# Kernel tuning notes

Hardware: AMD Instinct MI355X
Metric: run time of the kernel (lower is better)

## Reference

```python
import jax, jax.numpy as jnp
import numpy as np

V, L, H, D, DFF = 32000, 6, 8, 64, 1024
DM = H * D  # 512
N, T = 4, 1024
EPS = 1e-3  # keras LayerNormalization default epsilon


def setup_inputs() -> dict:
    key = jax.random.key(0)
    ks = jax.random.split(key, 13)
    s = 0.02
    return {
        "x": jax.random.randint(ks[0], (N, T), 0, V, dtype=jnp.int32),
        "emb": jax.random.normal(ks[1], (V, DM), jnp.float32) * s,
        "Wqkv": jax.random.normal(ks[2], (L, DM, 3 * DM), jnp.float32) * s,
        "bqkv": jnp.zeros((L, 3 * DM), jnp.float32),
        "Wff": jax.random.normal(ks[3], (L, DM, DFF), jnp.float32) * s,
        "bff": jnp.zeros((L, DFF), jnp.float32),
        "Wo": jax.random.normal(ks[4], (L, DFF, DM), jnp.float32) * s,
        "bo": jnp.zeros((L, DM), jnp.float32),
        "g1": jnp.ones((L, DM), jnp.float32),
        "beta1": jnp.zeros((L, DM), jnp.float32),
        "g2": jnp.ones((L, DM), jnp.float32),
        "beta2": jnp.zeros((L, DM), jnp.float32),
    }


def _pos_encoding(seq_len, d_model):
    pos = jnp.arange(seq_len, dtype=jnp.float32)[:, None]
    i = jnp.arange(d_model, dtype=jnp.float32)[None, :]
    angle_rates = 1.0 / jnp.power(10000.0, 2.0 * jnp.floor(i / 2.0) / d_model)
    ang = pos * angle_rates
    even = (jnp.arange(d_model) % 2) == 0
    return jnp.where(even[None, :], jnp.sin(ang), jnp.cos(ang))  # [T, DM]


def _ln(x, g, b):
    m = jnp.mean(x, axis=-1, keepdims=True)
    v = jnp.mean(jnp.square(x - m), axis=-1, keepdims=True)
    return g * (x - m) / jnp.sqrt(v + EPS) + b


def reference(x, emb, Wqkv, bqkv, Wff, bff, Wo, bo, g1, beta1, g2, beta2):
    n, t = x.shape
    h = emb[x] * jnp.sqrt(jnp.float32(DM))          # [N,T,DM]
    h = h + _pos_encoding(t, DM)[None, :, :]
    # causal additive mask: 1 above diagonal, 0 on/below
    mask = 1.0 - jnp.tril(jnp.ones((t, t), jnp.float32))
    neg = mask[None, None, :, :] * -1e9
    scale = 1.0 / jnp.sqrt(jnp.float32(D))
    for l in range(L):
        qkv = h @ Wqkv[l] + bqkv[l]                 # [N,T,3*DM]
        qkv = qkv.reshape(n, t, H, D, 3)
        q, k, v = [jnp.transpose(qkv[..., j], (0, 2, 1, 3)) for j in range(3)]  # [N,H,T,D]
        logits = jnp.einsum("nhtd,nhsd->nhts", q, k) * scale + neg
        w = jax.nn.softmax(logits, axis=-1)
        a = jnp.einsum("nhts,nhsd->nhtd", w, v)     # [N,H,T,D]
        a = jnp.transpose(a, (0, 2, 1, 3)).reshape(n, t, DM)
        h = _ln(h + a, g1[l], beta1[l])
        ff = jax.nn.relu(h @ Wff[l] + bff[l]) @ Wo[l] + bo[l]
        h = _ln(h + ff, g2[l], beta2[l])
    return h
```

## Files before the change

kernel.cpp:

```cpp
#include <hip/hip_runtime.h>
#include <hip/hip_bf16.h>
#include <math.h>

#define DM   512
#define TT   1024
#define NB   4
#define NHD  8
#define LAYERS 6
#define DFFD 1024
#define MROWS (NB*TT)
#define PERBUF (NB*NHD*TT*64)

typedef __bf16 bf16x8 __attribute__((ext_vector_type(8)));
typedef __bf16 bf16x4 __attribute__((ext_vector_type(4)));
typedef float f32x4 __attribute__((ext_vector_type(4)));

__device__ __forceinline__ void gl_lds16(const __bf16* g, __bf16* l) {
    __builtin_amdgcn_global_load_lds((const __attribute__((address_space(1))) void*)g,
                                     (__attribute__((address_space(3))) void*)l, 16, 0, 0);
}

__global__ __launch_bounds__(256) void embed_pos_kernel(const int* __restrict__ x,
    const float* __restrict__ emb, float* __restrict__ h, __bf16* __restrict__ hb)
{
    int row = blockIdx.x;
    int t = row & (TT - 1);
    int tok = x[row];
    const float* e = emb + (size_t)tok * DM;
    float* out = h + (size_t)row * DM;
    __bf16* outb = hb + (size_t)row * DM;
    for (int i = threadIdx.x; i < DM; i += 256) {
        float val = e[i] * 22.62741699796952f;
        int pair = i >> 1;
        float rate = powf(10000.0f, -(float)pair * (1.0f / 256.0f));
        float ang = (float)t * rate;
        float pe = (i & 1) ? cosf(ang) : sinf(ang);
        float v = val + pe;
        out[i] = v;
        outb[i] = (__bf16)v;
    }
}

__global__ __launch_bounds__(256) void convert_all_kernel(
    const float* __restrict__ Wqkv, const float* __restrict__ Wff, const float* __restrict__ Wo,
    const float* __restrict__ bqkv,
    __bf16* __restrict__ WtQ, __bf16* __restrict__ WtF, __bf16* __restrict__ WtO,
    float* __restrict__ bqkv_p)
{
    __shared__ float tile[32][33];
    int l = blockIdx.z;
    int t = blockIdx.x;
    const float* W; __bf16* Wt; int K, N, bx, by; bool perm = false;
    if (t < 768)       { W = Wqkv; Wt = WtQ; K = 512;  N = 1536; bx = t & 15;  by = t >> 4; perm = true; }
    else if (t < 1280) { int u = t - 768;  W = Wff; Wt = WtF; K = 512;  N = 1024; bx = u & 15; by = u >> 4; }
    else               { int u = t - 1280; W = Wo;  Wt = WtO; K = 1024; N = 512;  bx = u & 31; by = u >> 5; }
    int k0 = bx * 32, n0 = by * 32;
    const float* Wl = W + (size_t)l * K * N;
    __bf16* Wtl = Wt + (size_t)l * K * N;
    int tx = threadIdx.x & 31, ty = threadIdx.x >> 5;
    #pragma unroll
    for (int i = ty; i < 32; i += 8)
        tile[i][tx] = Wl[(size_t)(k0 + i) * N + n0 + tx];
    if (perm && bx == 0 && ty == 0) {
        int c = n0 + tx;
        bqkv_p[l * 1536 + (c % 3) * 512 + c / 3] = bqkv[(size_t)l * 1536 + c];
    }
    __syncthreads();
    #pragma unroll
    for (int i = ty; i < 32; i += 8) {
        int c = n0 + i;
        int row = perm ? ((c % 3) * 512 + c / 3) : c;
        Wtl[(size_t)row * K + k0 + tx] = (__bf16)tile[tx][i];
    }
}

__global__ __launch_bounds__(256) void gemm_mfma(const __bf16* __restrict__ A,
    const __bf16* __restrict__ Bt, const float* __restrict__ bias,
    __bf16* __restrict__ Cb, int M, int Nc, int K, int mode)
{
    __shared__ __align__(16) __bf16 As[2][128 * 32];
    __shared__ __align__(16) __bf16 Bs[2][128 * 32];
    int tid = threadIdx.x;
    int lane = tid & 63;
    int wave = tid >> 6;
    int ln = lane & 15, q = lane >> 4;
    int wrow = (wave >> 1) * 64, wcol = (wave & 1) * 64;
    int n0 = blockIdx.x * 128, m0 = blockIdx.y * 128;

    f32x4 acc[4][4] = {};

    const __bf16* Ab = A + (size_t)m0 * K;
    const __bf16* Bb = Bt + (size_t)n0 * K;

    int srow = lane >> 2;
    int scol = (lane & 3) * 8;
    const __bf16* Ag0 = Ab + (size_t)(wave * 32 + srow) * K + scol;
    const __bf16* Ag1 = Ab + (size_t)(wave * 32 + 16 + srow) * K + scol;
    const __bf16* Bg0 = Bb + (size_t)(wave * 32 + srow) * K + scol;
    const __bf16* Bg1 = Bb + (size_t)(wave * 32 + 16 + srow) * K + scol;

    for (int k0 = 0; k0 < K; k0 += 64) {
        __syncthreads();
        #pragma unroll
        for (int p = 0; p < 2; p++) {
            int kp = k0 + p * 32;
            gl_lds16(Ag0 + kp, As[p] + (wave * 32) * 32);
            gl_lds16(Ag1 + kp, As[p] + (wave * 32 + 16) * 32);
            gl_lds16(Bg0 + kp, Bs[p] + (wave * 32) * 32);
            gl_lds16(Bg1 + kp, Bs[p] + (wave * 32 + 16) * 32);
        }
        __syncthreads();

        #pragma unroll
        for (int p = 0; p < 2; p++) {
            bf16x8 af[4], bfr[4];
            #pragma unroll
            for (int mt = 0; mt < 4; mt++)
                af[mt] = *(const bf16x8*)&As[p][(wrow + mt * 16 + ln) * 32 + q * 8];
            #pragma unroll
            for (int nt = 0; nt < 4; nt++)
                bfr[nt] = *(const bf16x8*)&Bs[p][(wcol + nt * 16 + ln) * 32 + q * 8];
            #pragma unroll
            for (int mt = 0; mt < 4; mt++)
                #pragma unroll
                for (int nt = 0; nt < 4; nt++)
                    acc[mt][nt] = __builtin_amdgcn_mfma_f32_16x16x32_bf16(af[mt], bfr[nt], acc[mt][nt], 0, 0, 0);
        }
    }

    #pragma unroll
    for (int mt = 0; mt < 4; mt++) {
        int mbase = m0 + wrow + mt * 16 + q * 4;
        if (mode == 1) {
            #pragma unroll
            for (int r = 0; r < 4; r++) {
                int m = mbase + r;
                #pragma unroll
                for (int nt = 0; nt < 4; nt++) {
                    int c = n0 + wcol + nt * 16 + ln;
                    float val = acc[mt][nt][r] + bias[c];
                    Cb[(size_t)m * Nc + c] = (__bf16)fmaxf(val, 0.f);
                }
            }
        } else {
            int n = mbase >> 10, t = mbase & (TT - 1);
            #pragma unroll
            for (int nt = 0; nt < 4; nt++) {
                int c = n0 + wcol + nt * 16 + ln;
                int buf = c >> 9;
                int hd = c & 511;
                int hh = hd >> 6, d = hd & 63;
                float bv = bias[c];
                if (buf == 2) {
                    size_t idx = 2 * (size_t)PERBUF + (((size_t)(n * NHD + hh) * 64 + d) << 10) + t;
                    bf16x4 v4;
                    #pragma unroll
                    for (int r = 0; r < 4; r++) v4[r] = (__bf16)(acc[mt][nt][r] + bv);
                    *(bf16x4*)&Cb[idx] = v4;
                } else {
                    size_t base = (size_t)buf * PERBUF + (((size_t)(n * NHD + hh) * TT + t) << 6) + d;
                    #pragma unroll
                    for (int r = 0; r < 4; r++)
                        Cb[base + (size_t)(r << 6)] = (__bf16)(acc[mt][nt][r] + bv);
                }
            }
        }
    }
}

__global__ __launch_bounds__(256) void gemm_ff2(const __bf16* __restrict__ A,
    const __bf16* __restrict__ Bt, const float* __restrict__ bias,
    float* __restrict__ C, int M, int Nc, int K)
{
    __shared__ __align__(16) __bf16 As[2][128 * 32];
    __shared__ __align__(16) __bf16 Bs[2][64 * 32];
    int tid = threadIdx.x;
    int lane = tid & 63;
    int wave = tid >> 6;
    int ln = lane & 15, q = lane >> 4;
    int wrow = (wave >> 1) * 64, wcol = (wave & 1) * 32;
    int n0 = blockIdx.x * 64, m0 = blockIdx.y * 128;

    f32x4 acc[4][2] = {};

    const __bf16* Ab = A + (size_t)m0 * K;
    const __bf16* Bb = Bt + (size_t)n0 * K;

    int srow = lane >> 2;
    int scol = (lane & 3) * 8;
    const __bf16* Ag0 = Ab + (size_t)(wave * 32 + srow) * K + scol;
    const __bf16* Ag1 = Ab + (size_t)(wave * 32 + 16 + srow) * K + scol;
    const __bf16* Bg0 = Bb + (size_t)(wave * 16 + srow) * K + scol;

    for (int k0 = 0; k0 < K; k0 += 64) {
        __syncthreads();
        #pragma unroll
        for (int p = 0; p < 2; p++) {
            int kp = k0 + p * 32;
            gl_lds16(Ag0 + kp, As[p] + (wave * 32) * 32);
            gl_lds16(Ag1 + kp, As[p] + (wave * 32 + 16) * 32);
            gl_lds16(Bg0 + kp, Bs[p] + (wave * 16) * 32);
        }
        __syncthreads();

        #pragma unroll
        for (int p = 0; p < 2; p++) {
            bf16x8 af[4], bfr[2];
            #pragma unroll
            for (int mt = 0; mt < 4; mt++)
                af[mt] = *(const bf16x8*)&As[p][(wrow + mt * 16 + ln) * 32 + q * 8];
            #pragma unroll
            for (int nt = 0; nt < 2; nt++)
                bfr[nt] = *(const bf16x8*)&Bs[p][(wcol + nt * 16 + ln) * 32 + q * 8];
            #pragma unroll
            for (int mt = 0; mt < 4; mt++)
                #pragma unroll
                for (int nt = 0; nt < 2; nt++)
                    acc[mt][nt] = __builtin_amdgcn_mfma_f32_16x16x32_bf16(af[mt], bfr[nt], acc[mt][nt], 0, 0, 0);
        }
    }

    #pragma unroll
    for (int mt = 0; mt < 4; mt++) {
        #pragma unroll
        for (int r = 0; r < 4; r++) {
            int m = m0 + wrow + mt * 16 + q * 4 + r;
            #pragma unroll
            for (int nt = 0; nt < 2; nt++) {
                int c = n0 + wcol + nt * 16 + ln;
                C[(size_t)m * Nc + c] = acc[mt][nt][r] + bias[c];
            }
        }
    }
}

#define PPAD 72
#define NCHUNK 40
__global__ __launch_bounds__(256) void attn_partial_kernel(const __bf16* __restrict__ qb,
    const __bf16* __restrict__ kb, const __bf16* __restrict__ vtb,
    float* __restrict__ po, float* __restrict__ pden)
{
    __shared__ __align__(16) __bf16 Ksh[64 * 64];
    __shared__ __align__(16) __bf16 Vsh[2][64 * 64];
    __shared__ __align__(16) __bf16 Ps[64 * PPAD];

    int u = (NCHUNK - 1) - blockIdx.x;
    int nh = blockIdx.y;
    int g, off;
    if (u < 4)       { g = 0; off = 0;  }
    else if (u < 12) { g = 1; off = 4;  }
    else if (u < 24) { g = 2; off = 12; }
    else             { g = 3; off = 24; }
    int rem = u - off;
    int nper = g + 1;
    int qq = rem / nper;
    int c  = rem - qq * nper;
    int qt = g * 4 + qq;
    int st0 = c * 4;
    int st1 = min(st0 + 4, qt + 1);

    int tid = threadIdx.x;
    int lane = tid & 63, w = tid >> 6;
    int ln = lane & 15, q = lane >> 4;

    const __bf16* Kg = kb + (size_t)nh * TT * 64;
    const __bf16* Vg = vtb + (size_t)nh * 64 * TT;

    const __bf16* Qrow = qb + ((size_t)nh * TT + (size_t)qt * 64 + w * 16 + ln) * 64;
    bf16x8 aq0 = *(const bf16x8*)(Qrow + q * 8);
    bf16x8 aq1 = *(const bf16x8*)(Qrow + 32 + q * 8);

    int srow = lane >> 3;
    int swz  = ((lane & 7) ^ srow) << 3;
    int r0 = (w * 2 + 0) * 8 + srow;
    int r1 = (w * 2 + 1) * 8 + srow;
    const __bf16* Kg0 = Kg + (size_t)r0 * 64 + swz;
    const __bf16* Kg1 = Kg + (size_t)r1 * 64 + swz;
    const __bf16* Vg0 = Vg + (size_t)r0 * TT + swz;
    const __bf16* Vg1 = Vg + (size_t)r1 * TT + swz;
    __bf16* Kd0 = Ksh + (w * 2 + 0) * 512;
    __bf16* Kd1 = Ksh + (w * 2 + 1) * 512;

    f32x4 o_acc[4] = {};
    float den_reg[4] = {0.f, 0.f, 0.f, 0.f};

    int cur = 0;
    gl_lds16(Kg0 + st0 * 4096, Kd0);
    gl_lds16(Kg1 + st0 * 4096, Kd1);
    gl_lds16(Vg0 + st0 * 64, Vsh[0] + (w * 2 + 0) * 512);
    gl_lds16(Vg1 + st0 * 64, Vsh[0] + (w * 2 + 1) * 512);

    int kswz = ln & 7;
    for (int st = st0; st < st1; st++) {
        __syncthreads();

        f32x4 s_acc[4] = {};
        #pragma unroll
        for (int nt = 0; nt < 4; nt++) {
            int r = nt * 16 + ln;
            bf16x8 b0 = *(const bf16x8*)&Ksh[r * 64 + ((q ^ kswz) << 3)];
            s_acc[nt] = __builtin_amdgcn_mfma_f32_16x16x32_bf16(aq0, b0, s_acc[nt], 0, 0, 0);
            bf16x8 b1 = *(const bf16x8*)&Ksh[r * 64 + (((q + 4) ^ kswz) << 3)];
            s_acc[nt] = __builtin_amdgcn_mfma_f32_16x16x32_bf16(aq1, b1, s_acc[nt], 0, 0, 0);
        }

        bool diag = (st == qt);
        #pragma unroll
        for (int nt = 0; nt < 4; nt++) {
            #pragma unroll
            for (int r = 0; r < 4; r++) {
                int lrow = w * 16 + q * 4 + r;
                int lcol = nt * 16 + ln;
                float p;
                if (diag && lcol > lrow) p = 0.f;
                else p = exp2f(s_acc[nt][r] * 0.18033688011112042f);
                den_reg[r] += p;
                Ps[lrow * PPAD + lcol] = (__bf16)p;
            }
        }
        __syncthreads();

        if (st + 1 < st1) {
            gl_lds16(Kg0 + (st + 1) * 4096, Kd0);
            gl_lds16(Kg1 + (st + 1) * 4096, Kd1);
            gl_lds16(Vg0 + (st + 1) * 64, Vsh[cur ^ 1] + (w * 2 + 0) * 512);
            gl_lds16(Vg1 + (st + 1) * 64, Vsh[cur ^ 1] + (w * 2 + 1) * 512);
        }

        #pragma unroll
        for (int ks = 0; ks < 2; ks++) {
            bf16x8 af = *(const bf16x8*)&Vsh[cur][(w * 16 + ln) * 64 + (((ks * 4 + q) ^ kswz) << 3)];
            #pragma unroll
            for (int nt = 0; nt < 4; nt++) {
                bf16x8 bfr = *(const bf16x8*)&Ps[(nt * 16 + ln) * PPAD + ks * 32 + q * 8];
                o_acc[nt] = __builtin_amdgcn_mfma_f32_16x16x32_bf16(af, bfr, o_acc[nt], 0, 0, 0);
            }
        }
        cur ^= 1;
    }

    #pragma unroll
    for (int m = 1; m < 16; m <<= 1)
        #pragma unroll
        for (int r = 0; r < 4; r++)
            den_reg[r] += __shfl_xor(den_reg[r], m, 64);
    size_t slot = (size_t)nh * NCHUNK + u;
    if (ln == 0)
        #pragma unroll
        for (int r = 0; r < 4; r++)
            pden[slot * 64 + w * 16 + q * 4 + r] = den_reg[r];

    #pragma unroll
    for (int nt = 0; nt < 4; nt++)
        *(f32x4*)&po[(slot << 12) + (size_t)(nt * 16 + ln) * 64 + w * 16 + q * 4] = o_acc[nt];
}

__global__ __launch_bounds__(256) void add_ln_attn_kernel(float* __restrict__ h,
    __bf16* __restrict__ hb, const float* __restrict__ po, const float* __restrict__ pden,
    const float* __restrict__ g, const float* __restrict__ b)
{
    int w = threadIdx.x >> 6, lane = threadIdx.x & 63;
    int row = (blockIdx.x << 2) + w;
    int n = row >> 10, t = row & (TT - 1);
    int qt = t >> 6, qrow = t & 63;
    int gg = qt >> 2, nc = gg + 1;
    const int offs[4] = {0, 4, 12, 24};
    int u0 = offs[gg] + (qt - gg * 4) * nc;
    int hh = lane >> 3;
    int d0 = (lane & 7) * 8;
    size_t s0 = (size_t)(n * NHD + hh) * NCHUNK + u0;

    f32x4 a0 = {0.f,0.f,0.f,0.f}, a1 = {0.f,0.f,0.f,0.f};
    float den = 0.f;
    for (int c = 0; c < nc; c++) {
        const float* p = po + ((s0 + c) << 12) + (size_t)qrow * 64 + d0;
        a0 += *(const f32x4*)p;
        a1 += *(const f32x4*)(p + 4);
        den += pden[(s0 + c) * 64 + qrow];
    }
    float inv = 1.0f / den;

    size_t base = (size_t)row * DM + lane * 8;
    f32x4 x0 = *(const f32x4*)&h[base];
    f32x4 x1 = *(const f32x4*)&h[base + 4];
    x0 += a0 * inv;
    x1 += a1 * inv;

    float s1 = x0[0]+x0[1]+x0[2]+x0[3] + x1[0]+x1[1]+x1[2]+x1[3];
    float s2 = x0[0]*x0[0]+x0[1]*x0[1]+x0[2]*x0[2]+x0[3]*x0[3]
             + x1[0]*x1[0]+x1[1]*x1[1]+x1[2]*x1[2]+x1[3]*x1[3];
    #pragma unroll
    for (int m = 1; m < 64; m <<= 1) {
        s1 += __shfl_xor(s1, m, 64);
        s2 += __shfl_xor(s2, m, 64);
    }
    float mean = s1 * (1.0f / 512.0f);
    float var = s2 * (1.0f / 512.0f) - mean * mean;
    float rstd = rsqrtf(var + 1e-3f);

    f32x4 gg0 = *(const f32x4*)&g[lane * 8];
    f32x4 gg1 = *(const f32x4*)&g[lane * 8 + 4];
    f32x4 bb0 = *(const f32x4*)&b[lane * 8];
    f32x4 bb1 = *(const f32x4*)&b[lane * 8 + 4];
    f32x4 o0, o1;
    bf16x8 pb;
    #pragma unroll
    for (int i = 0; i < 4; i++) {
        o0[i] = gg0[i] * ((x0[i] - mean) * rstd) + bb0[i];
        o1[i] = gg1[i] * ((x1[i] - mean) * rstd) + bb1[i];
        pb[i] = (__bf16)o0[i];
        pb[4 + i] = (__bf16)o1[i];
    }
    *(f32x4*)&h[base] = o0;
    *(f32x4*)&h[base + 4] = o1;
    *(bf16x8*)(hb + base) = pb;
}

__global__ __launch_bounds__(256) void add_ln_kernel(float* __restrict__ h,
    __bf16* __restrict__ hb, const float* __restrict__ a,
    const float* __restrict__ g, const float* __restrict__ b)
{
    int w = threadIdx.x >> 6, lane = threadIdx.x & 63;
    int row = (blockIdx.x << 2) + w;
    size_t base4 = (size_t)row * (DM / 4);
    const float4* h4 = (const float4*)h;
    const float4* a4 = (const float4*)a;
    float4 x0 = h4[base4 + lane];
    float4 x1 = h4[base4 + 64 + lane];
    float4 y0 = a4[base4 + lane];
    float4 y1 = a4[base4 + 64 + lane];
    x0.x += y0.x; x0.y += y0.y; x0.z += y0.z; x0.w += y0.w;
    x1.x += y1.x; x1.y += y1.y; x1.z += y1.z; x1.w += y1.w;
    float s1 = x0.x + x0.y + x0.z + x0.w + x1.x + x1.y + x1.z + x1.w;
    float s2 = x0.x*x0.x + x0.y*x0.y + x0.z*x0.z + x0.w*x0.w
             + x1.x*x1.x + x1.y*x1.y + x1.z*x1.z + x1.w*x1.w;
    #pragma unroll
    for (int m = 1; m < 64; m <<= 1) {
        s1 += __shfl_xor(s1, m, 64);
        s2 += __shfl_xor(s2, m, 64);
    }
    float mean = s1 * (1.0f / 512.0f);
    float var = s2 * (1.0f / 512.0f) - mean * mean;
    float rstd = rsqrtf(var + 1e-3f);
    const float4* g4 = (const float4*)g;
    const float4* b4 = (const float4*)b;
    float4 gg0 = g4[lane], gg1 = g4[64 + lane];
    float4 bb0 = b4[lane], bb1 = b4[64 + lane];
    float4 o0, o1;
    o0.x = gg0.x * ((x0.x - mean) * rstd) + bb0.x;
    o0.y = gg0.y * ((x0.y - mean) * rstd) + bb0.y;
    o0.z = gg0.z * ((x0.z - mean) * rstd) + bb0.z;
    o0.w = gg0.w * ((x0.w - mean) * rstd) + bb0.w;
    o1.x = gg1.x * ((x1.x - mean) * rstd) + bb1.x;
    o1.y = gg1.y * ((x1.y - mean) * rstd) + bb1.y;
    o1.z = gg1.z * ((x1.z - mean) * rstd) + bb1.z;
    o1.w = gg1.w * ((x1.w - mean) * rstd) + bb1.w;
    ((float4*)h)[base4 + lane] = o0;
    ((float4*)h)[base4 + 64 + lane] = o1;
    bf16x4 p0, p1;
    p0[0] = (__bf16)o0.x; p0[1] = (__bf16)o0.y; p0[2] = (__bf16)o0.z; p0[3] = (__bf16)o0.w;
    p1[0] = (__bf16)o1.x; p1[1] = (__bf16)o1.y; p1[2] = (__bf16)o1.z; p1[3] = (__bf16)o1.w;
    *(bf16x4*)(hb + (size_t)row * DM + lane * 4) = p0;
    *(bf16x4*)(hb + (size_t)row * DM + 256 + lane * 4) = p1;
}

extern "C" void kernel_launch(void* const* d_in, const int* in_sizes, int n_in,
                              void* d_out, int out_size, void* d_ws, size_t ws_size,
                              hipStream_t stream) {
    const int*   x     = (const int*)d_in[0];
    const float* emb   = (const float*)d_in[1];
    const float* Wqkv  = (const float*)d_in[2];
    const float* bqkv  = (const float*)d_in[3];
    const float* Wff   = (const float*)d_in[4];
    const float* bff   = (const float*)d_in[5];
    const float* Wo    = (const float*)d_in[6];
    const float* bo    = (const float*)d_in[7];
    const float* g1    = (const float*)d_in[8];
    const float* beta1 = (const float*)d_in[9];
    const float* g2    = (const float*)d_in[10];
    const float* beta2 = (const float*)d_in[11];

    float* h = (float*)d_out;
    char* w = (char*)d_ws;
    __bf16* qkvb = (__bf16*)w;
    __bf16* ffb  = (__bf16*)w;
    float*  abuf = (float*)(w + 25165824);
    __bf16* hb   = (__bf16*)(w + 33554432);
    __bf16* WtQ  = (__bf16*)(w + 37748736);
    __bf16* WtF  = (__bf16*)(w + 47185920);
    __bf16* WtO  = (__bf16*)(w + 53477376);
    float*  po   = (float*)(w + 59768832);
    float*  pden = (float*)(w + 80740352);
    float*  bqkv_p = (float*)(w + 81068032);

    convert_all_kernel<<<dim3(1792, 1, LAYERS), 256, 0, stream>>>(
        Wqkv, Wff, Wo, bqkv, WtQ, WtF, WtO, bqkv_p);

    embed_pos_kernel<<<MROWS, 256, 0, stream>>>(x, emb, h, hb);

    for (int l = 0; l < LAYERS; l++) {
        const float* bff_l  = bff  + (size_t)l * DFFD;
        const float* bo_l   = bo   + (size_t)l * DM;

        gemm_mfma<<<dim3(12, 32), 256, 0, stream>>>(
            hb, WtQ + (size_t)l * 1536 * 512, bqkv_p + l * 1536, qkvb, MROWS, 3 * DM, DM, 2);

        attn_partial_kernel<<<dim3(NCHUNK, NB * NHD), 256, 0, stream>>>(
            qkvb, qkvb + PERBUF, qkvb + 2 * (size_t)PERBUF, po, pden);

        add_ln_attn_kernel<<<MROWS / 4, 256, 0, stream>>>(
            h, hb, po, pden, g1 + l * DM, beta1 + l * DM);

        gemm_mfma<<<dim3(8, 32), 256, 0, stream>>>(
            hb, WtF + (size_t)l * 1024 * 512, bff_l, ffb, MROWS, DFFD, DM, 1);

        gemm_ff2<<<dim3(8, 32), 256, 0, stream>>>(
            ffb, WtO + (size_t)l * 512 * 1024, bo_l, abuf, MROWS, DM, DFFD);

        add_ln_kernel<<<MROWS / 4, 256, 0, stream>>>(h, hb, abuf, g2 + l * DM, beta2 + l * DM);
    }
}
```

Baseline: 672.9 us.

## Replace split-KV partial attention with one block per query tile and in-kernel normalization

Attention no longer splits each query tile's key range into chunks of up to four key tiles written to partial-output and denominator buffers. Each block now handles one whole (batch·head, query tile) pair over all causal key tiles, with query tiles ordered heavy-to-light, and normalizes by the row sum inside the kernel. This removes the partial-sum buffers and the reduction loop in the add+LayerNorm kernel, cutting global traffic. In exchange there are fewer blocks (512 vs 1280), and the longest blocks run 16 key tiles serially, which risks load imbalance and lower parallelism.

```diff
diff --git a/kernel.cpp b/kernel.cpp
--- a/kernel.cpp
+++ b/kernel.cpp
@@ -235,29 +235,19 @@
 }
 
 #define PPAD 72
-#define NCHUNK 40
-__global__ __launch_bounds__(256) void attn_partial_kernel(const __bf16* __restrict__ qb,
+__global__ __launch_bounds__(256) void attn_kernel(const __bf16* __restrict__ qb,
     const __bf16* __restrict__ kb, const __bf16* __restrict__ vtb,
-    float* __restrict__ po, float* __restrict__ pden)
+    float* __restrict__ o)
 {
     __shared__ __align__(16) __bf16 Ksh[64 * 64];
     __shared__ __align__(16) __bf16 Vsh[2][64 * 64];
     __shared__ __align__(16) __bf16 Ps[64 * PPAD];
-
-    int u = (NCHUNK - 1) - blockIdx.x;
-    int nh = blockIdx.y;
-    int g, off;
-    if (u < 4)       { g = 0; off = 0;  }
-    else if (u < 12) { g = 1; off = 4;  }
-    else if (u < 24) { g = 2; off = 12; }
-    else             { g = 3; off = 24; }
-    int rem = u - off;
-    int nper = g + 1;
-    int qq = rem / nper;
-    int c  = rem - qq * nper;
-    int qt = g * 4 + qq;
-    int st0 = c * 4;
-    int st1 = min(st0 + 4, qt + 1);
+    __shared__ float Ds[64];
+
+    int nh = blockIdx.x;
+    int u  = blockIdx.y;
+    int qt = (u < 8) ? (15 - u) : (u - 8);
+    int st1 = qt + 1;
 
     int tid = threadIdx.x;
     int lane = tid & 63, w = tid >> 6;
@@ -285,13 +275,13 @@
     float den_reg[4] = {0.f, 0.f, 0.f, 0.f};
 
     int cur = 0;
-    gl_lds16(Kg0 + st0 * 4096, Kd0);
-    gl_lds16(Kg1 + st0 * 4096, Kd1);
-    gl_lds16(Vg0 + st0 * 64, Vsh[0] + (w * 2 + 0) * 512);
-    gl_lds16(Vg1 + st0 * 64, Vsh[0] + (w * 2 + 1) * 512);
+    gl_lds16(Kg0, Kd0);
+    gl_lds16(Kg1, Kd1);
+    gl_lds16(Vg0, Vsh[0] + (w * 2 + 0) * 512);
+    gl_lds16(Vg1, Vsh[0] + (w * 2 + 1) * 512);
 
     int kswz = ln & 7;
-    for (int st = st0; st < st1; st++) {
+    for (int st = 0; st < st1; st++) {
         __syncthreads();
 
         f32x4 s_acc[4] = {};
@@ -344,47 +334,41 @@
         #pragma unroll
         for (int r = 0; r < 4; r++)
             den_reg[r] += __shfl_xor(den_reg[r], m, 64);
-    size_t slot = (size_t)nh * NCHUNK + u;
     if (ln == 0)
         #pragma unroll
         for (int r = 0; r < 4; r++)
-            pden[slot * 64 + w * 16 + q * 4 + r] = den_reg[r];
-
-    #pragma unroll
-    for (int nt = 0; nt < 4; nt++)
-        *(f32x4*)&po[(slot << 12) + (size_t)(nt * 16 + ln) * 64 + w * 16 + q * 4] = o_acc[nt];
+            Ds[w * 16 + q * 4 + r] = den_reg[r];
+    __syncthreads();
+
+    size_t obase = ((size_t)nh * 16 + qt) << 12;
+    #pragma unroll
+    for (int nt = 0; nt < 4; nt++) {
+        float inv = 1.0f / Ds[nt * 16 + ln];
+        f32x4 v = o_acc[nt];
+        v *= inv;
+        *(f32x4*)&o[obase + (size_t)(nt * 16 + ln) * 64 + w * 16 + q * 4] = v;
+    }
 }
 
 __global__ __launch_bounds__(256) void add_ln_attn_kernel(float* __restrict__ h,
-    __bf16* __restrict__ hb, const float* __restrict__ po, const float* __restrict__ pden,
+    __bf16* __restrict__ hb, const float* __restrict__ o,
     const float* __restrict__ g, const float* __restrict__ b)
 {
     int w = threadIdx.x >> 6, lane = threadIdx.x & 63;
     int row = (blockIdx.x << 2) + w;
     int n = row >> 10, t = row & (TT - 1);
     int qt = t >> 6, qrow = t & 63;
-    int gg = qt >> 2, nc = gg + 1;
-    const int offs[4] = {0, 4, 12, 24};
-    int u0 = offs[gg] + (qt - gg * 4) * nc;
     int hh = lane >> 3;
     int d0 = (lane & 7) * 8;
-    size_t s0 = (size_t)(n * NHD + hh) * NCHUNK + u0;
-
-    f32x4 a0 = {0.f,0.f,0.f,0.f}, a1 = {0.f,0.f,0.f,0.f};
-    float den = 0.f;
-    for (int c = 0; c < nc; c++) {
-        const float* p = po + ((s0 + c) << 12) + (size_t)qrow * 64 + d0;
-        a0 += *(const f32x4*)p;
-        a1 += *(const f32x4*)(p + 4);
-        den += pden[(s0 + c) * 64 + qrow];
-    }
-    float inv = 1.0f / den;
+    const float* p = o + ((((size_t)(n * NHD + hh) * 16 + qt) << 12) + (size_t)qrow * 64 + d0);
+    f32x4 a0 = *(const f32x4*)p;
+    f32x4 a1 = *(const f32x4*)(p + 4);
 
     size_t base = (size_t)row * DM + lane * 8;
     f32x4 x0 = *(const f32x4*)&h[base];
     f32x4 x1 = *(const f32x4*)&h[base + 4];
-    x0 += a0 * inv;
-    x1 += a1 * inv;
+    x0 += a0;
+    x1 += a1;
 
     float s1 = x0[0]+x0[1]+x0[2]+x0[3] + x1[0]+x1[1]+x1[2]+x1[3];
     float s2 = x0[0]*x0[0]+x0[1]*x0[1]+x0[2]*x0[2]+x0[3]*x0[3]
@@ -489,9 +473,8 @@
     __bf16* WtQ  = (__bf16*)(w + 37748736);
     __bf16* WtF  = (__bf16*)(w + 47185920);
     __bf16* WtO  = (__bf16*)(w + 53477376);
-    float*  po   = (float*)(w + 59768832);
-    float*  pden = (float*)(w + 80740352);
-    float*  bqkv_p = (float*)(w + 81068032);
+    float*  attno = (float*)(w + 59768832);
+    float*  bqkv_p = (float*)(w + 80740352);
 
     convert_all_kernel<<<dim3(1792, 1, LAYERS), 256, 0, stream>>>(
         Wqkv, Wff, Wo, bqkv, WtQ, WtF, WtO, bqkv_p);
@@ -505,11 +488,11 @@
         gemm_mfma<<<dim3(12, 32), 256, 0, stream>>>(
             hb, WtQ + (size_t)l * 1536 * 512, bqkv_p + l * 1536, qkvb, MROWS, 3 * DM, DM, 2);
 
-        attn_partial_kernel<<<dim3(NCHUNK, NB * NHD), 256, 0, stream>>>(
-            qkvb, qkvb + PERBUF, qkvb + 2 * (size_t)PERBUF, po, pden);
+        attn_kernel<<<dim3(32, 16), 256, 0, stream>>>(
+            qkvb, qkvb + PERBUF, qkvb + 2 * (size_t)PERBUF, attno);
 
         add_ln_attn_kernel<<<MROWS / 4, 256, 0, stream>>>(
-            h, hb, po, pden, g1 + l * DM, beta1 + l * DM);
+            h, hb, attno, g1 + l * DM, beta1 + l * DM);
 
         gemm_mfma<<<dim3(8, 32), 256, 0, stream>>>(
             hb, WtF + (size_t)l * 1024 * 512, bff_l, ffb, MROWS, DFFD, DM, 1);
```

After: 689.1 us. 2.4% more time.

## Double-buffer GEMM K-loop so LDS loads overlap MFMA compute

Applied to the files above, without the earlier changes.

Both bf16 GEMM kernels now use software pipelining. The next 32-wide K slice is loaded into the alternate LDS buffer while MFMAs run on the current one, with a prologue and epilogue around the loop. Previously all loads finished behind a barrier before any compute began. This adds one barrier per 32-wide slice and relies on the async global_load_lds completing by the next barrier.

```diff
diff --git a/kernel.cpp b/kernel.cpp
--- a/kernel.cpp
+++ b/kernel.cpp
@@ -99,34 +99,42 @@
     const __bf16* Bg0 = Bb + (size_t)(wave * 32 + srow) * K + scol;
     const __bf16* Bg1 = Bb + (size_t)(wave * 32 + 16 + srow) * K + scol;
 
-    for (int k0 = 0; k0 < K; k0 += 64) {
+    auto STAGE = [&](int kp, int buf) {
+        gl_lds16(Ag0 + kp, As[buf] + (wave * 32) * 32);
+        gl_lds16(Ag1 + kp, As[buf] + (wave * 32 + 16) * 32);
+        gl_lds16(Bg0 + kp, Bs[buf] + (wave * 32) * 32);
+        gl_lds16(Bg1 + kp, Bs[buf] + (wave * 32 + 16) * 32);
+    };
+    auto COMPUTE = [&](int buf) {
+        bf16x8 af[4], bfr[4];
+        #pragma unroll
+        for (int mt = 0; mt < 4; mt++)
+            af[mt] = *(const bf16x8*)&As[buf][(wrow + mt * 16 + ln) * 32 + q * 8];
+        #pragma unroll
+        for (int nt = 0; nt < 4; nt++)
+            bfr[nt] = *(const bf16x8*)&Bs[buf][(wcol + nt * 16 + ln) * 32 + q * 8];
+        #pragma unroll
+        for (int mt = 0; mt < 4; mt++)
+            #pragma unroll
+            for (int nt = 0; nt < 4; nt++)
+                acc[mt][nt] = __builtin_amdgcn_mfma_f32_16x16x32_bf16(af[mt], bfr[nt], acc[mt][nt], 0, 0, 0);
+    };
+
+    STAGE(0, 0);
+    __syncthreads();
+    int kp = 0;
+    for (; kp + 64 < K; kp += 64) {
+        STAGE(kp + 32, 1);
+        COMPUTE(0);
         __syncthreads();
-        #pragma unroll
-        for (int p = 0; p < 2; p++) {
-            int kp = k0 + p * 32;
-            gl_lds16(Ag0 + kp, As[p] + (wave * 32) * 32);
-            gl_lds16(Ag1 + kp, As[p] + (wave * 32 + 16) * 32);
-            gl_lds16(Bg0 + kp, Bs[p] + (wave * 32) * 32);
-            gl_lds16(Bg1 + kp, Bs[p] + (wave * 32 + 16) * 32);
-        }
+        STAGE(kp + 64, 0);
+        COMPUTE(1);
         __syncthreads();
-
-        #pragma unroll
-        for (int p = 0; p < 2; p++) {
-            bf16x8 af[4], bfr[4];
-            #pragma unroll
-            for (int mt = 0; mt < 4; mt++)
-                af[mt] = *(const bf16x8*)&As[p][(wrow + mt * 16 + ln) * 32 + q * 8];
-            #pragma unroll
-            for (int nt = 0; nt < 4; nt++)
-                bfr[nt] = *(const bf16x8*)&Bs[p][(wcol + nt * 16 + ln) * 32 + q * 8];
-            #pragma unroll
-            for (int mt = 0; mt < 4; mt++)
-                #pragma unroll
-                for (int nt = 0; nt < 4; nt++)
-                    acc[mt][nt] = __builtin_amdgcn_mfma_f32_16x16x32_bf16(af[mt], bfr[nt], acc[mt][nt], 0, 0, 0);
-        }
-    }
+    }
+    STAGE(kp + 32, 1);
+    COMPUTE(0);
+    __syncthreads();
+    COMPUTE(1);
 
     #pragma unroll
     for (int mt = 0; mt < 4; mt++) {
@@ -192,33 +200,41 @@
     const __bf16* Ag1 = Ab + (size_t)(wave * 32 + 16 + srow) * K + scol;
     const __bf16* Bg0 = Bb + (size_t)(wave * 16 + srow) * K + scol;
 
-    for (int k0 = 0; k0 < K; k0 += 64) {
+    auto STAGE = [&](int kp, int buf) {
+        gl_lds16(Ag0 + kp, As[buf] + (wave * 32) * 32);
+        gl_lds16(Ag1 + kp, As[buf] + (wave * 32 + 16) * 32);
+        gl_lds16(Bg0 + kp, Bs[buf] + (wave * 16) * 32);
+    };
+    auto COMPUTE = [&](int buf) {
+        bf16x8 af[4], bfr[2];
+        #pragma unroll
+        for (int mt = 0; mt < 4; mt++)
+            af[mt] = *(const bf16x8*)&As[buf][(wrow + mt * 16 + ln) * 32 + q * 8];
+        #pragma unroll
+        for (int nt = 0; nt < 2; nt++)
+            bfr[nt] = *(const bf16x8*)&Bs[buf][(wcol + nt * 16 + ln) * 32 + q * 8];
+        #pragma unroll
+        for (int mt = 0; mt < 4; mt++)
+            #pragma unroll
+            for (int nt = 0; nt < 2; nt++)
+                acc[mt][nt] = __builtin_amdgcn_mfma_f32_16x16x32_bf16(af[mt], bfr[nt], acc[mt][nt], 0, 0, 0);
+    };
+
+    STAGE(0, 0);
+    __syncthreads();
+    int kp = 0;
+    for (; kp + 64 < K; kp += 64) {
+        STAGE(kp + 32, 1);
+        COMPUTE(0);
         __syncthreads();
-        #pragma unroll
-        for (int p = 0; p < 2; p++) {
-            int kp = k0 + p * 32;
-            gl_lds16(Ag0 + kp, As[p] + (wave * 32) * 32);
-            gl_lds16(Ag1 + kp, As[p] + (wave * 32 + 16) * 32);
-            gl_lds16(Bg0 + kp, Bs[p] + (wave * 16) * 32);
-        }
+        STAGE(kp + 64, 0);
+        COMPUTE(1);
         __syncthreads();
-
-        #pragma unroll
-        for (int p = 0; p < 2; p++) {
-            bf16x8 af[4], bfr[2];
-            #pragma unroll
-            for (int mt = 0; mt < 4; mt++)
-                af[mt] = *(const bf16x8*)&As[p][(wrow + mt * 16 + ln) * 32 + q * 8];
-            #pragma unroll
-            for (int nt = 0; nt < 2; nt++)
-                bfr[nt] = *(const bf16x8*)&Bs[p][(wcol + nt * 16 + ln) * 32 + q * 8];
-            #pragma unroll
-            for (int mt = 0; mt < 4; mt++)
-                #pragma unroll
-                for (int nt = 0; nt < 2; nt++)
-                    acc[mt][nt] = __builtin_amdgcn_mfma_f32_16x16x32_bf16(af[mt], bfr[nt], acc[mt][nt], 0, 0, 0);
-        }
-    }
+    }
+    STAGE(kp + 32, 1);
+    COMPUTE(0);
+    __syncthreads();
+    COMPUTE(1);
 
     #pragma unroll
     for (int mt = 0; mt < 4; mt++) {
```

Result: no change. 670.3 us (-0.4%).

## Load GEMM operand fragments directly from global memory, bypassing LDS staging

Applied to the files above, without the earlier changes.

Both MFMA GEMM kernels drop their shared-memory tiles and the global_load_lds staging with its two barriers per K step. Each wave now reads its A and B fragments straight from global memory into registers. This removes barrier synchronisation and LDS traffic, but the two waves sharing a row or column now fetch the same data separately through cache. It also loses the coalesced staging pattern and any overlap between loads and compute, since there is no prefetch.

```diff
diff --git a/kernel.cpp b/kernel.cpp
--- a/kernel.cpp
+++ b/kernel.cpp
@@ -78,8 +78,6 @@
     const __bf16* __restrict__ Bt, const float* __restrict__ bias,
     __bf16* __restrict__ Cb, int M, int Nc, int K, int mode)
 {
-    __shared__ __align__(16) __bf16 As[2][128 * 32];
-    __shared__ __align__(16) __bf16 Bs[2][128 * 32];
     int tid = threadIdx.x;
     int lane = tid & 63;
     int wave = tid >> 6;
@@ -89,43 +87,22 @@
 
     f32x4 acc[4][4] = {};
 
-    const __bf16* Ab = A + (size_t)m0 * K;
-    const __bf16* Bb = Bt + (size_t)n0 * K;
-
-    int srow = lane >> 2;
-    int scol = (lane & 3) * 8;
-    const __bf16* Ag0 = Ab + (size_t)(wave * 32 + srow) * K + scol;
-    const __bf16* Ag1 = Ab + (size_t)(wave * 32 + 16 + srow) * K + scol;
-    const __bf16* Bg0 = Bb + (size_t)(wave * 32 + srow) * K + scol;
-    const __bf16* Bg1 = Bb + (size_t)(wave * 32 + 16 + srow) * K + scol;
-
-    for (int k0 = 0; k0 < K; k0 += 64) {
-        __syncthreads();
-        #pragma unroll
-        for (int p = 0; p < 2; p++) {
-            int kp = k0 + p * 32;
-            gl_lds16(Ag0 + kp, As[p] + (wave * 32) * 32);
-            gl_lds16(Ag1 + kp, As[p] + (wave * 32 + 16) * 32);
-            gl_lds16(Bg0 + kp, Bs[p] + (wave * 32) * 32);
-            gl_lds16(Bg1 + kp, Bs[p] + (wave * 32 + 16) * 32);
-        }
-        __syncthreads();
-
-        #pragma unroll
-        for (int p = 0; p < 2; p++) {
-            bf16x8 af[4], bfr[4];
-            #pragma unroll
-            for (int mt = 0; mt < 4; mt++)
-                af[mt] = *(const bf16x8*)&As[p][(wrow + mt * 16 + ln) * 32 + q * 8];
+    const __bf16* Arow0 = A  + (size_t)(m0 + wrow + ln) * K + q * 8;
+    const __bf16* Brow0 = Bt + (size_t)(n0 + wcol + ln) * K + q * 8;
+
+    for (int kp = 0; kp < K; kp += 32) {
+        bf16x8 af[4], bfr[4];
+        #pragma unroll
+        for (int mt = 0; mt < 4; mt++)
+            af[mt] = *(const bf16x8*)(Arow0 + (size_t)(mt * 16) * K + kp);
+        #pragma unroll
+        for (int nt = 0; nt < 4; nt++)
+            bfr[nt] = *(const bf16x8*)(Brow0 + (size_t)(nt * 16) * K + kp);
+        #pragma unroll
+        for (int mt = 0; mt < 4; mt++)
             #pragma unroll
             for (int nt = 0; nt < 4; nt++)
-                bfr[nt] = *(const bf16x8*)&Bs[p][(wcol + nt * 16 + ln) * 32 + q * 8];
-            #pragma unroll
-            for (int mt = 0; mt < 4; mt++)
-                #pragma unroll
-                for (int nt = 0; nt < 4; nt++)
-                    acc[mt][nt] = __builtin_amdgcn_mfma_f32_16x16x32_bf16(af[mt], bfr[nt], acc[mt][nt], 0, 0, 0);
-        }
+                acc[mt][nt] = __builtin_amdgcn_mfma_f32_16x16x32_bf16(af[mt], bfr[nt], acc[mt][nt], 0, 0, 0);
     }
 
     #pragma unroll
@@ -172,8 +149,6 @@
     const __bf16* __restrict__ Bt, const float* __restrict__ bias,
     float* __restrict__ C, int M, int Nc, int K)
 {
-    __shared__ __align__(16) __bf16 As[2][128 * 32];
-    __shared__ __align__(16) __bf16 Bs[2][64 * 32];
     int tid = threadIdx.x;
     int lane = tid & 63;
     int wave = tid >> 6;
@@ -183,41 +158,22 @@
 
     f32x4 acc[4][2] = {};
 
-    const __bf16* Ab = A + (size_t)m0 * K;
-    const __bf16* Bb = Bt + (size_t)n0 * K;
-
-    int srow = lane >> 2;
-    int scol = (lane & 3) * 8;
-    const __bf16* Ag0 = Ab + (size_t)(wave * 32 + srow) * K + scol;
-    const __bf16* Ag1 = Ab + (size_t)(wave * 32 + 16 + srow) * K + scol;
-    const __bf16* Bg0 = Bb + (size_t)(wave * 16 + srow) * K + scol;
-
-    for (int k0 = 0; k0 < K; k0 += 64) {
-        __syncthreads();
-        #pragma unroll
-        for (int p = 0; p < 2; p++) {
-            int kp = k0 + p * 32;
-            gl_lds16(Ag0 + kp, As[p] + (wave * 32) * 32);
-            gl_lds16(Ag1 + kp, As[p] + (wave * 32 + 16) * 32);
-            gl_lds16(Bg0 + kp, Bs[p] + (wave * 16) * 32);
-        }
-        __syncthreads();
-
-        #pragma unroll
-        for (int p = 0; p < 2; p++) {
-            bf16x8 af[4], bfr[2];
-            #pragma unroll
-            for (int mt = 0; mt < 4; mt++)
-                af[mt] = *(const bf16x8*)&As[p][(wrow + mt * 16 + ln) * 32 + q * 8];
+    const __bf16* Arow0 = A  + (size_t)(m0 + wrow + ln) * K + q * 8;
+    const __bf16* Brow0 = Bt + (size_t)(n0 + wcol + ln) * K + q * 8;
+
+    for (int kp = 0; kp < K; kp += 32) {
+        bf16x8 af[4], bfr[2];
+        #pragma unroll
+        for (int mt = 0; mt < 4; mt++)
+            af[mt] = *(const bf16x8*)(Arow0 + (size_t)(mt * 16) * K + kp);
+        #pragma unroll
+        for (int nt = 0; nt < 2; nt++)
+            bfr[nt] = *(const bf16x8*)(Brow0 + (size_t)(nt * 16) * K + kp);
+        #pragma unroll
+        for (int mt = 0; mt < 4; mt++)
             #pragma unroll
             for (int nt = 0; nt < 2; nt++)
-                bfr[nt] = *(const bf16x8*)&Bs[p][(wcol + nt * 16 + ln) * 32 + q * 8];
-            #pragma unroll
-            for (int mt = 0; mt < 4; mt++)
-                #pragma unroll
-                for (int nt = 0; nt < 2; nt++)
-                    acc[mt][nt] = __builtin_amdgcn_mfma_f32_16x16x32_bf16(af[mt], bfr[nt], acc[mt][nt], 0, 0, 0);
-        }
+                acc[mt][nt] = __builtin_amdgcn_mfma_f32_16x16x32_bf16(af[mt], bfr[nt], acc[mt][nt], 0, 0, 0);
     }
 
     #pragma unroll
```

New measurement: 827.8 us. 1.23x slower.
